# Kernel optimization log

Hardware: AMD Instinct MI355X
Metric: run time of the kernel (lower is better)

## Reference

```python
import jax, jax.numpy as jnp
import numpy as np

EPS = 1e-5
NUM_GRAPHS = 1000


def _glorot(key, shape):
    fan_in, fan_out = shape[1], shape[0]
    lim = float(np.sqrt(6.0 / (fan_in + fan_out)))
    return jax.random.uniform(key, shape, jnp.float32, -lim, lim)


def setup_inputs() -> dict:
    N, E, C, D, L = 100_000, 1_600_000, 10_000, 32, 4
    key = jax.random.key(0)
    ks = jax.random.split(key, 12)
    x = jax.random.normal(ks[0], (N, 2), jnp.float32)
    edge_index = jax.random.randint(ks[1], (2, E), 0, N)
    edge_attr = jax.random.normal(ks[2], (E, 1), jnp.float32)
    candidate_idxs = jax.random.randint(ks[3], (C,), 0, N)
    batch = jnp.sort(jax.random.randint(ks[4], (N,), 0, NUM_GRAPHS))
    lk = jax.random.split(ks[5], L)
    lk2 = jax.random.split(ks[6], L)
    return {
        "x": x,
        "edge_index": edge_index,
        "edge_attr": edge_attr,
        "candidate_idxs": candidate_idxs,
        "batch": batch,
        "lin_in_w": _glorot(ks[7], (D, 2)),
        "lin_in_b": jnp.zeros((D,), jnp.float32),
        "w1": jnp.stack([_glorot(lk[i], (D, 2 * D + 1)) for i in range(L)]),
        "b1": jnp.zeros((L, D), jnp.float32),
        "bn1_g": jnp.ones((L, D), jnp.float32),
        "bn1_b": jnp.zeros((L, D), jnp.float32),
        "w2": jnp.stack([_glorot(lk2[i], (D, D)) for i in range(L)]),
        "b2": jnp.zeros((L, D), jnp.float32),
        "bn2_g": jnp.ones((L, D), jnp.float32),
        "bn2_b": jnp.zeros((L, D), jnp.float32),
        "lin_out_w": _glorot(ks[8], (1, D)),
        "lin_out_b": jnp.zeros((), jnp.float32),
    }


def _batchnorm(m, g, b):
    # training-mode BatchNorm1d over the edge (row) axis, biased variance
    mu = jnp.mean(m, axis=0)
    var = jnp.mean(jnp.square(m - mu), axis=0)
    return (m - mu) * jax.lax.rsqrt(var + EPS) * g + b


def reference(x, edge_index, edge_attr, candidate_idxs, batch,
              lin_in_w, lin_in_b, w1, b1, bn1_g, bn1_b,
              w2, b2, bn2_g, bn2_b, lin_out_w, lin_out_b):
    N = x.shape[0]
    src, dst = edge_index[0], edge_index[1]  # x_j = x[src], x_i = x[dst]
    h = x @ lin_in_w.T + lin_in_b  # [N, D]
    for l in range(w1.shape[0]):
        msg = jnp.concatenate([h[dst], h[src], edge_attr], axis=-1)  # [E, 2D+1]
        m = jax.nn.relu(_batchnorm(msg @ w1[l].T + b1[l], bn1_g[l], bn1_b[l]))
        m = jax.nn.relu(_batchnorm(m @ w2[l].T + b2[l], bn2_g[l], bn2_b[l]))
        h = h + jax.ops.segment_sum(m, dst, num_segments=N)
    logits = (h[candidate_idxs] @ lin_out_w.T)[:, 0] + lin_out_b  # [C]
    seg = batch[candidate_idxs]
    mx = jax.ops.segment_max(logits, seg, num_segments=NUM_GRAPHS)
    mx = jnp.where(jnp.isfinite(mx), mx, 0.0)
    lse = mx + jnp.log(jax.ops.segment_sum(jnp.exp(logits - mx[seg]), seg,
                                           num_segments=NUM_GRAPHS))
    return logits - lse[seg]
```

## Files before the change

### kernel.cpp

```cpp
#include <hip/hip_runtime.h>
#include <stdint.h>

#define NGRAPH 1000

typedef __attribute__((ext_vector_type(8))) short short8;
typedef __attribute__((ext_vector_type(4))) float f32x4;

static __device__ __forceinline__ uint32_t pack2_bf16(float a, float b) {
  uint32_t ua = __float_as_uint(a), ub = __float_as_uint(b);
  ua = (ua + 0x7fffu + ((ua >> 16) & 1u)) >> 16;
  ub = (ub + 0x7fffu + ((ub >> 16) & 1u)) >> 16;
  return ua | (ub << 16);
}
static __device__ __forceinline__ unsigned short f2bf(float x) {
  uint32_t u = __float_as_uint(x);
  u = (u + 0x7fffu + ((u >> 16) & 1u)) >> 16;
  return (unsigned short)u;
}
static __device__ __forceinline__ float bf2f(unsigned short u) {
  return __uint_as_float(((uint32_t)u) << 16);
}
union frag_u { short8 v; uint32_t u[4]; };

__global__ __launch_bounds__(256) void k_prep(const float* __restrict__ w1,
                                              float* __restrict__ w1n,
                                              float* __restrict__ w1c) {
  int t = blockIdx.x * 256 + threadIdx.x;
  if (t < 4 * 2048) {
    int l = t >> 11, r = t & 2047, k = r >> 6, o = r & 63;
    w1n[t] = (o < 32) ? w1[l * 2080 + o * 65 + k]
                      : w1[l * 2080 + (o - 32) * 65 + (k + 32)];
  } else if (t < 4 * 2048 + 4 * 32) {
    int u = t - 4 * 2048;
    int l = u >> 5, d = u & 31;
    w1c[u] = w1[l * 2080 + d * 65 + 64];
  }
}

__global__ __launch_bounds__(256) void k_init(const float* __restrict__ x,
                                              const float* __restrict__ wi,
                                              const float* __restrict__ bi,
                                              float* __restrict__ h, int N) {
  int t = blockIdx.x * 256 + threadIdx.x;
  if (t >= N * 32) return;
  int n = t >> 5, d = t & 31;
  h[t] = fmaf(x[2 * n], wi[2 * d], fmaf(x[2 * n + 1], wi[2 * d + 1], bi[d]));
}

__global__ __launch_bounds__(256) void k_zero32(int* __restrict__ p, int n) {
  int t = blockIdx.x * 256 + threadIdx.x;
  if (t < n) p[t] = 0;
}

#define CHUNK 2048
__global__ __launch_bounds__(256) void k_bucket(const int* __restrict__ src,
                                                const int* __restrict__ dst,
                                                const float* __restrict__ ea,
                                                int* __restrict__ gcur,
                                                int* __restrict__ cnt,
                                                uint32_t* __restrict__ b0,
                                                uint32_t* __restrict__ b1,
                                                int E, int pstep, int cap) {
  __shared__ int lcnt[8], lbase[8];
  const int t = threadIdx.x;
  const int base = blockIdx.x * CHUNK;
  if (t < 8) lcnt[t] = 0;
  __syncthreads();
  int ps[8];
  uint32_t w0[8], w1[8];
#pragma unroll
  for (int j = 0; j < 8; j++) {
    int e = base + j * 256 + t;
    bool ok = e < E;
    int d = ok ? dst[e] : 0;
    int s = ok ? src[e] : 0;
    float eav = ok ? ea[e] : 0.f;
    int g = d / pstep;
    ps[j] = ok ? g : -1;
    if (ok) {
      int rank = atomicAdd(cnt + d, 1);
      w0[j] = ((uint32_t)s << 14) | (uint32_t)(rank & 16383);
      w1[j] = ((uint32_t)(d - g * pstep) << 16) | (uint32_t)f2bf(eav);
      atomicAdd(&lcnt[g], 1);
    }
  }
  __syncthreads();
  if (t < 8) lbase[t] = atomicAdd(&gcur[t], lcnt[t]);
  __syncthreads();
  if (t < 8) lcnt[t] = lbase[t];
  __syncthreads();
#pragma unroll
  for (int j = 0; j < 8; j++) {
    if (ps[j] >= 0) {
      int pos = atomicAdd(&lcnt[ps[j]], 1);
      if (pos < cap) {
        size_t idx = (size_t)ps[j] * cap + pos;
        b0[idx] = w0[j];
        b1[idx] = w1[j];
      }
    }
  }
}

__global__ __launch_bounds__(256) void k_scan1(const int* __restrict__ in,
                                               int* __restrict__ out,
                                               int* __restrict__ bsum, int n) {
  __shared__ int sh[256];
  const int t = threadIdx.x;
  const int idx = blockIdx.x * 1024 + t * 4;
  int v[4];
#pragma unroll
  for (int j = 0; j < 4; j++) v[j] = (idx + j < n) ? in[idx + j] : 0;
  int tsum = v[0] + v[1] + v[2] + v[3];
  sh[t] = tsum;
  __syncthreads();
#pragma unroll
  for (int ofs = 1; ofs < 256; ofs <<= 1) {
    int x = (t >= ofs) ? sh[t - ofs] : 0;
    __syncthreads();
    sh[t] += x;
    __syncthreads();
  }
  int run = sh[t] - tsum;
  if (t == 255) bsum[blockIdx.x] = sh[255];
#pragma unroll
  for (int j = 0; j < 4; j++) {
    if (idx + j < n) out[idx + j] = run;
    run += v[j];
  }
}
__global__ __launch_bounds__(256) void k_scan2(int* __restrict__ bsum, int nb) {
  __shared__ int sh[256];
  const int t = threadIdx.x;
  int val = (t < nb) ? bsum[t] : 0;
  sh[t] = val;
  __syncthreads();
#pragma unroll
  for (int ofs = 1; ofs < 256; ofs <<= 1) {
    int x = (t >= ofs) ? sh[t - ofs] : 0;
    __syncthreads();
    sh[t] += x;
    __syncthreads();
  }
  if (t < nb) bsum[t] = sh[t] - val;
}
__global__ __launch_bounds__(256) void k_scan3(int* __restrict__ rowptr,
                                               const int* __restrict__ bsum, int n) {
  int t = blockIdx.x * 256 + threadIdx.x;
  if (t >= n) return;
  rowptr[t] = rowptr[t] + bsum[t >> 10];
}

__global__ __launch_bounds__(256) void k_node(const float* __restrict__ h,
                                              const float* __restrict__ w1n,
                                              unsigned short* __restrict__ hAB, int N) {
  const int wid = (blockIdx.x * 256 + threadIdx.x) >> 6;
  const int lane = threadIdx.x & 63;
  if (wid >= N) return;
  const int n = __builtin_amdgcn_readfirstlane(wid);
  const float* hn = h + (size_t)n * 32;
  float acc = 0.f;
#pragma unroll
  for (int k = 0; k < 32; k++) acc = fmaf(hn[k], w1n[k * 64 + lane], acc);
  hAB[(size_t)n * 64 + lane] = f2bf(acc);
}

__global__ __launch_bounds__(256) void k_combine(
    const uint32_t* __restrict__ hAB, const uint32_t* __restrict__ b0,
    const uint32_t* __restrict__ b1, const int* __restrict__ gcur,
    const int* __restrict__ rowptr, const float* __restrict__ w1c,
    uint32_t* __restrict__ mpre, float* __restrict__ stats, int pstep, int cap) {
  const int t = threadIdx.x;
  const int r = t & 3;
  float ssum[8], ssq[8];
#pragma unroll
  for (int q = 0; q < 8; q++) { ssum[q] = 0.f; ssq[q] = 0.f; }
  float wc[8];
#pragma unroll
  for (int j = 0; j < 8; j++) wc[j] = w1c[8 * r + j];

  const int gstride = (gridDim.x * blockDim.x) >> 2;
  const int eg0 = (blockIdx.x * blockDim.x + t) >> 2;
  for (int g = 0; g < 8; g++) {
    const int len = gcur[g];
    const size_t o = (size_t)g * cap;
    for (int i = eg0; i < len; i += gstride) {
      const uint32_t w0 = b0[o + i];
      const uint32_t w1 = b1[o + i];
      const int vs = (int)(w0 >> 14);
      const int rank = (int)(w0 & 16383u);
      const int d = g * pstep + (int)(w1 >> 16);
      const float eav = bf2f((unsigned short)(w1 & 0xffffu));
      const int pos = rowptr[d] + rank;
      const uint4 av = *(const uint4*)(hAB + (size_t)d * 32 + r * 4);
      const uint4 bv = *(const uint4*)(hAB + (size_t)vs * 32 + 16 + r * 4);
      const uint32_t ad[4] = {av.x, av.y, av.z, av.w};
      const uint32_t bd[4] = {bv.x, bv.y, bv.z, bv.w};
      float m[8];
#pragma unroll
      for (int p = 0; p < 4; p++) {
        float a0 = __uint_as_float(ad[p] << 16), a1 = __uint_as_float(ad[p] & 0xffff0000u);
        float bb0 = __uint_as_float(bd[p] << 16), bb1 = __uint_as_float(bd[p] & 0xffff0000u);
        m[2 * p]     = a0 + fmaf(eav, wc[2 * p],     bb0);
        m[2 * p + 1] = a1 + fmaf(eav, wc[2 * p + 1], bb1);
      }
      uint4 out = make_uint4(pack2_bf16(m[0], m[1]), pack2_bf16(m[2], m[3]),
                             pack2_bf16(m[4], m[5]), pack2_bf16(m[6], m[7]));
      *(uint4*)(mpre + (size_t)pos * 16 + r * 4) = out;
#pragma unroll
      for (int q = 0; q < 8; q++) { ssum[q] += m[q]; ssq[q] = fmaf(m[q], m[q], ssq[q]); }
    }
  }
#pragma unroll
  for (int q = 0; q < 8; q++) {
#pragma unroll
    for (int msk = 4; msk <= 32; msk <<= 1) {
      ssum[q] += __shfl_xor(ssum[q], msk, 64);
      ssq[q]  += __shfl_xor(ssq[q],  msk, 64);
    }
  }
  __shared__ float red[4][64];
  const int lane = t & 63, wv = t >> 6;
  if (lane < 4) {
#pragma unroll
    for (int j = 0; j < 8; j++) {
      red[wv][lane * 8 + j]      = ssum[j];
      red[wv][32 + lane * 8 + j] = ssq[j];
    }
  }
  __syncthreads();
  if (t < 64)
    stats[(size_t)blockIdx.x * 64 + t] = red[0][t] + red[1][t] + red[2][t] + red[3][t];
}

__global__ __launch_bounds__(256) void k_finalize(const float* __restrict__ stats, int nblk, int E,
                                                  const float* __restrict__ g,
                                                  const float* __restrict__ bb,
                                                  float* __restrict__ ss) {
  const int q = blockIdx.x;
  const int t = threadIdx.x;
  double s0 = 0.0, s1 = 0.0;
  for (int i = t; i < nblk; i += 256) {
    s0 += (double)stats[(size_t)i * 64 + q];
    s1 += (double)stats[(size_t)i * 64 + 32 + q];
  }
  __shared__ double r0[256], r1[256];
  r0[t] = s0; r1[t] = s1;
  __syncthreads();
#pragma unroll
  for (int m = 128; m >= 1; m >>= 1) {
    if (t < m) { r0[t] += r0[t + m]; r1[t] += r1[t + m]; }
    __syncthreads();
  }
  if (t == 0) {
    double invE = 1.0 / (double)E;
    double mu = r0[0] * invE;
    double var = r1[0] * invE - mu * mu;
    if (var < 0.0) var = 0.0;
    double sc = (double)g[q] / sqrt(var + 1e-5);
    ss[q] = (float)sc;
    ss[32 + q] = (float)((double)bb[q] - mu * sc);
  }
}

__global__ __launch_bounds__(256) void k_gemm2m(
    uint32_t* __restrict__ mpre, const float* __restrict__ ss,
    const float* __restrict__ w2, float* __restrict__ stats, int E) {
  const int lane = threadIdx.x & 63;
  const int wv = threadIdx.x >> 6;
  const int row = lane & 15;
  const int kb = (lane >> 4) * 8;
  const int G = E >> 4;
  const int gstart = blockIdx.x * 4 + wv;
  const int gstride = gridDim.x * 4;

  float sc[8], sh[8];
#pragma unroll
  for (int j = 0; j < 8; j++) { sc[j] = ss[kb + j]; sh[j] = ss[32 + kb + j]; }

  frag_u b0, b1;
#pragma unroll
  for (int p = 0; p < 4; p++) {
    const float* wp0 = w2 + (size_t)row * 32 + kb + 2 * p;
    const float* wp1 = w2 + (size_t)(row + 16) * 32 + kb + 2 * p;
    b0.u[p] = pack2_bf16(wp0[0], wp0[1]);
    b1.u[p] = pack2_bf16(wp1[0], wp1[1]);
  }

  float sum0 = 0.f, sq0 = 0.f, sum1 = 0.f, sq1 = 0.f;
  unsigned short* mp16 = (unsigned short*)mpre;

  for (int g = gstart; g < G; g += gstride) {
    const int e0 = g << 4;
    const uint4 raw = *(const uint4*)(mpre + (size_t)(e0 + row) * 16 + (lane >> 4) * 4);
    float m[8];
    m[0] = __uint_as_float(raw.x << 16); m[1] = __uint_as_float(raw.x & 0xffff0000u);
    m[2] = __uint_as_float(raw.y << 16); m[3] = __uint_as_float(raw.y & 0xffff0000u);
    m[4] = __uint_as_float(raw.z << 16); m[5] = __uint_as_float(raw.z & 0xffff0000u);
    m[6] = __uint_as_float(raw.w << 16); m[7] = __uint_as_float(raw.w & 0xffff0000u);
    frag_u a;
#pragma unroll
    for (int p = 0; p < 4; p++) {
      float x0 = fmaxf(fmaf(m[2 * p],     sc[2 * p],     sh[2 * p]),     0.f);
      float x1 = fmaxf(fmaf(m[2 * p + 1], sc[2 * p + 1], sh[2 * p + 1]), 0.f);
      a.u[p] = pack2_bf16(x0, x1);
    }
    f32x4 z = {0.f, 0.f, 0.f, 0.f};
    f32x4 acc0 = __builtin_amdgcn_mfma_f32_16x16x32_bf16(a.v, b0.v, z, 0, 0, 0);
    f32x4 acc1 = __builtin_amdgcn_mfma_f32_16x16x32_bf16(a.v, b1.v, z, 0, 0, 0);
#pragma unroll
    for (int r = 0; r < 4; r++) {
      sum0 += acc0[r]; sq0 = fmaf(acc0[r], acc0[r], sq0);
      sum1 += acc1[r]; sq1 = fmaf(acc1[r], acc1[r], sq1);
      const size_t base = (size_t)(e0 + (lane >> 4) * 4 + r) * 32;
      mp16[base + row]      = f2bf(acc0[r]);
      mp16[base + row + 16] = f2bf(acc1[r]);
    }
  }

  sum0 += __shfl_xor(sum0, 16); sum0 += __shfl_xor(sum0, 32);
  sq0  += __shfl_xor(sq0, 16);  sq0  += __shfl_xor(sq0, 32);
  sum1 += __shfl_xor(sum1, 16); sum1 += __shfl_xor(sum1, 32);
  sq1  += __shfl_xor(sq1, 16);  sq1  += __shfl_xor(sq1, 32);
  __shared__ float red[4][64];
  if (lane < 16) {
    red[wv][row] = sum0;      red[wv][16 + row] = sum1;
    red[wv][32 + row] = sq0;  red[wv][48 + row] = sq1;
  }
  __syncthreads();
  if (threadIdx.x < 64) {
    int q = threadIdx.x;
    stats[(size_t)blockIdx.x * 64 + q] = red[0][q] + red[1][q] + red[2][q] + red[3][q];
  }
}

__global__ __launch_bounds__(256) void k_agg(
    const unsigned short* __restrict__ mp16, const int* __restrict__ rowptr,
    const int* __restrict__ cnt, const float* __restrict__ ss,
    float* __restrict__ h, int N) {
  const int n = blockIdx.x * 8 + (threadIdx.x >> 5);
  if (n >= N) return;
  const int d = threadIdx.x & 31;
  const int start = rowptr[n];
  const int deg = cnt[n];
  const float sc = ss[d], sh = ss[32 + d];
  const unsigned short* p = mp16 + (size_t)start * 32 + d;
  float acc = 0.f;
  int j = 0;
  for (; j + 2 <= deg; j += 2) {
    float x0 = bf2f(p[(size_t)j * 32]);
    float x1 = bf2f(p[(size_t)(j + 1) * 32]);
    acc += fmaxf(fmaf(x0, sc, sh), 0.f);
    acc += fmaxf(fmaf(x1, sc, sh), 0.f);
  }
  if (j < deg) {
    float x0 = bf2f(p[(size_t)j * 32]);
    acc += fmaxf(fmaf(x0, sc, sh), 0.f);
  }
  h[(size_t)n * 32 + d] += acc;
}

__global__ __launch_bounds__(256) void k_initseg(unsigned* __restrict__ segmax,
                                                 float* __restrict__ segsum) {
  int t = blockIdx.x * 256 + threadIdx.x;
  if (t < NGRAPH) { segmax[t] = 0u; segsum[t] = 0.f; }
}

__global__ __launch_bounds__(256) void k_logits(
    const float* __restrict__ h, const int* __restrict__ cand, const int* __restrict__ batch,
    const float* __restrict__ wout, const float* __restrict__ bout,
    float* __restrict__ logits, int* __restrict__ seg, unsigned* __restrict__ segmax, int C) {
  int t = blockIdx.x * 256 + threadIdx.x;
  if (t >= C) return;
  int node = cand[t];
  const float4* hp = (const float4*)(h + (size_t)node * 32);
  float acc = bout[0];
#pragma unroll
  for (int kc = 0; kc < 8; kc++) {
    float4 v = hp[kc];
    acc = fmaf(v.x, wout[kc * 4 + 0], acc);
    acc = fmaf(v.y, wout[kc * 4 + 1], acc);
    acc = fmaf(v.z, wout[kc * 4 + 2], acc);
    acc = fmaf(v.w, wout[kc * 4 + 3], acc);
  }
  logits[t] = acc;
  int s = batch[node];
  seg[t] = s;
  unsigned o = __float_as_uint(acc);
  o ^= (o >> 31) ? 0xFFFFFFFFu : 0x80000000u;
  atomicMax(segmax + s, o);
}

static __device__ __forceinline__ float o2f(unsigned o) {
  o ^= (o & 0x80000000u) ? 0x80000000u : 0xFFFFFFFFu;
  return __uint_as_float(o);
}

__global__ __launch_bounds__(256) void k_expsum(const float* __restrict__ logits,
                                                const int* __restrict__ seg,
                                                const unsigned* __restrict__ segmax,
                                                float* __restrict__ segsum, int C) {
  int t = blockIdx.x * 256 + threadIdx.x;
  if (t >= C) return;
  int s = seg[t];
  float mx = o2f(segmax[s]);
  atomicAdd(segsum + s, expf(logits[t] - mx));
}

__global__ __launch_bounds__(256) void k_out(const float* __restrict__ logits,
                                             const int* __restrict__ seg,
                                             const unsigned* __restrict__ segmax,
                                             const float* __restrict__ segsum,
                                             float* __restrict__ out, int C) {
  int t = blockIdx.x * 256 + threadIdx.x;
  if (t >= C) return;
  int s = seg[t];
  out[t] = logits[t] - (o2f(segmax[s]) + logf(segsum[s]));
}

extern "C" void kernel_launch(void* const* d_in, const int* in_sizes, int n_in,
                              void* d_out, int out_size, void* d_ws, size_t ws_size,
                              hipStream_t stream) {
  const float* x     = (const float*)d_in[0];
  const int*   eidx  = (const int*)d_in[1];
  const float* eattr = (const float*)d_in[2];
  const int*   cand  = (const int*)d_in[3];
  const int*   batch = (const int*)d_in[4];
  const float* wi    = (const float*)d_in[5];
  const float* bi    = (const float*)d_in[6];
  const float* w1    = (const float*)d_in[7];
  const float* g1    = (const float*)d_in[9];
  const float* bb1   = (const float*)d_in[10];
  const float* w2    = (const float*)d_in[11];
  const float* g2    = (const float*)d_in[13];
  const float* bb2   = (const float*)d_in[14];
  const float* wout  = (const float*)d_in[15];
  const float* bout  = (const float*)d_in[16];

  const int N = in_sizes[4];
  const int E = in_sizes[2];
  const int C = in_sizes[3];
  const int* src  = eidx;
  const int* dstp = eidx + E;

  char* ws = (char*)d_ws;
  size_t off = 0;
  auto carve = [&](size_t bytes) {
    void* p = ws + off;
    off = (off + bytes + 255) & ~(size_t)255;
    return p;
  };
  const int NBLK = 1024;
  const int pstep = (N + 7) / 8;
  const int cap = E / 8 + 8192;
  uint32_t* mpre   = (uint32_t*)carve((size_t)E * 64);
  float*    h      = (float*)carve((size_t)N * 32 * 4);
  uint32_t* hAB    = (uint32_t*)carve((size_t)N * 128);
  float*    w1n    = (float*)carve(4 * 2048 * 4);
  float*    w1c    = (float*)carve(4 * 32 * 4);
  float*    ss     = (float*)carve(64 * 4);
  float*    stats  = (float*)carve((size_t)NBLK * 64 * 4);
  int*      cnt    = (int*)carve((size_t)N * 4);
  int*      rowptr = (int*)carve((size_t)N * 4);
  int*      bsum   = (int*)carve(256 * 4);
  int*      gcur   = (int*)carve(8 * 4);
  uint32_t* b0     = (uint32_t*)carve((size_t)8 * cap * 4);
  uint32_t* b1buf  = (uint32_t*)carve((size_t)8 * cap * 4);
  float*    logits = (float*)carve((size_t)C * 4);
  int*      seg    = (int*)carve((size_t)C * 4);
  unsigned* segmax = (unsigned*)carve(NGRAPH * 4);
  float*    segsum = (float*)carve(NGRAPH * 4);
  (void)ws_size; (void)n_in; (void)out_size;

  const int nb1 = (N + 1023) / 1024;
  k_zero32<<<(N + 255) / 256, 256, 0, stream>>>(cnt, N);
  k_zero32<<<1, 256, 0, stream>>>(gcur, 8);
  k_bucket<<<(E + CHUNK - 1) / CHUNK, 256, 0, stream>>>(src, dstp, eattr, gcur, cnt,
                                                        b0, b1buf, E, pstep, cap);
  k_scan1<<<nb1, 256, 0, stream>>>(cnt, rowptr, bsum, N);
  k_scan2<<<1, 256, 0, stream>>>(bsum, nb1);
  k_scan3<<<(N + 255) / 256, 256, 0, stream>>>(rowptr, bsum, N);

  k_prep<<<33, 256, 0, stream>>>(w1, w1n, w1c);
  k_init<<<(N * 32 + 255) / 256, 256, 0, stream>>>(x, wi, bi, h, N);

  for (int l = 0; l < 4; l++) {
    k_node<<<(N * 64 + 255) / 256, 256, 0, stream>>>(h, w1n + l * 2048,
                                                     (unsigned short*)hAB, N);
    k_combine<<<NBLK, 256, 0, stream>>>(hAB, b0, b1buf, gcur, rowptr, w1c + l * 32,
                                        mpre, stats, pstep, cap);
    k_finalize<<<32, 256, 0, stream>>>(stats, NBLK, E, g1 + l * 32, bb1 + l * 32, ss);
    k_gemm2m<<<NBLK, 256, 0, stream>>>(mpre, ss, w2 + l * 1024, stats, E);
    k_finalize<<<32, 256, 0, stream>>>(stats, NBLK, E, g2 + l * 32, bb2 + l * 32, ss);
    k_agg<<<(N + 7) / 8, 256, 0, stream>>>((const unsigned short*)mpre, rowptr, cnt,
                                           ss, h, N);
  }

  k_initseg<<<(NGRAPH + 255) / 256, 256, 0, stream>>>(segmax, segsum);
  k_logits<<<(C + 255) / 256, 256, 0, stream>>>(h, cand, batch, wout, bout,
                                                logits, seg, segmax, C);
  k_expsum<<<(C + 255) / 256, 256, 0, stream>>>(logits, seg, segmax, segsum, C);
  k_out<<<(C + 255) / 256, 256, 0, stream>>>(logits, seg, segmax, segsum, (float*)d_out, C);
}
```

Baseline: 781.5 us.

## Fuse aggregation with next-layer node projection and split edge loop across half-waves

Merges the per-layer aggregation kernel with the following node projection (h @ W1 halves), so the updated h feeds the next layer's hAB computation without a separate launch and re-read. Each node now uses a full 64-lane wave, with the two halves splitting the edge loop and combining by shuffle. The k_bucket chunk is also halved, and the zero kernels are replaced with hipMemsetAsync. The fused kernel does more work per node (32 shuffles plus FMAs) and uses half-idle lanes for the h store.

```diff
diff --git a/kernel.cpp b/kernel.cpp
--- a/kernel.cpp
+++ b/kernel.cpp
@@ -47,12 +47,7 @@
   h[t] = fmaf(x[2 * n], wi[2 * d], fmaf(x[2 * n + 1], wi[2 * d + 1], bi[d]));
 }
 
-__global__ __launch_bounds__(256) void k_zero32(int* __restrict__ p, int n) {
-  int t = blockIdx.x * 256 + threadIdx.x;
-  if (t < n) p[t] = 0;
-}
-
-#define CHUNK 2048
+#define CHUNK 1024
 __global__ __launch_bounds__(256) void k_bucket(const int* __restrict__ src,
                                                 const int* __restrict__ dst,
                                                 const float* __restrict__ ea,
@@ -66,10 +61,10 @@
   const int base = blockIdx.x * CHUNK;
   if (t < 8) lcnt[t] = 0;
   __syncthreads();
-  int ps[8];
-  uint32_t w0[8], w1[8];
-#pragma unroll
-  for (int j = 0; j < 8; j++) {
+  int ps[4];
+  uint32_t w0[4], w1[4];
+#pragma unroll
+  for (int j = 0; j < 4; j++) {
     int e = base + j * 256 + t;
     bool ok = e < E;
     int d = ok ? dst[e] : 0;
@@ -90,7 +85,7 @@
   if (t < 8) lcnt[t] = lbase[t];
   __syncthreads();
 #pragma unroll
-  for (int j = 0; j < 8; j++) {
+  for (int j = 0; j < 4; j++) {
     if (ps[j] >= 0) {
       int pos = atomicAdd(&lcnt[ps[j]], 1);
       if (pos < cap) {
@@ -334,30 +329,34 @@
   }
 }
 
-__global__ __launch_bounds__(256) void k_agg(
+__global__ __launch_bounds__(256) void k_aggnode(
     const unsigned short* __restrict__ mp16, const int* __restrict__ rowptr,
     const int* __restrict__ cnt, const float* __restrict__ ss,
-    float* __restrict__ h, int N) {
-  const int n = blockIdx.x * 8 + (threadIdx.x >> 5);
-  if (n >= N) return;
-  const int d = threadIdx.x & 31;
+    float* __restrict__ h, const float* __restrict__ w1n,
+    unsigned short* __restrict__ hAB, int N, int last) {
+  const int wid = (blockIdx.x * 256 + threadIdx.x) >> 6;
+  const int lane = threadIdx.x & 63;
+  if (wid >= N) return;
+  const int n = __builtin_amdgcn_readfirstlane(wid);
+  const int d = lane & 31, half = lane >> 5;
   const int start = rowptr[n];
   const int deg = cnt[n];
-  const float sc = ss[d], sh = ss[32 + d];
+  const float scv = ss[d], shv = ss[32 + d];
   const unsigned short* p = mp16 + (size_t)start * 32 + d;
   float acc = 0.f;
-  int j = 0;
-  for (; j + 2 <= deg; j += 2) {
-    float x0 = bf2f(p[(size_t)j * 32]);
-    float x1 = bf2f(p[(size_t)(j + 1) * 32]);
-    acc += fmaxf(fmaf(x0, sc, sh), 0.f);
-    acc += fmaxf(fmaf(x1, sc, sh), 0.f);
-  }
-  if (j < deg) {
-    float x0 = bf2f(p[(size_t)j * 32]);
-    acc += fmaxf(fmaf(x0, sc, sh), 0.f);
-  }
-  h[(size_t)n * 32 + d] += acc;
+  for (int j = half; j < deg; j += 2) {
+    float x = bf2f(p[(size_t)j * 32]);
+    acc += fmaxf(fmaf(x, scv, shv), 0.f);
+  }
+  acc += __shfl_xor(acc, 32, 64);
+  const float hnew = h[(size_t)n * 32 + d] + acc;
+  if (lane < 32) h[(size_t)n * 32 + lane] = hnew;
+  if (last) return;
+  float acc2 = 0.f;
+#pragma unroll
+  for (int k = 0; k < 32; k++)
+    acc2 = fmaf(__shfl(hnew, k, 64), w1n[k * 64 + lane], acc2);
+  hAB[(size_t)n * 64 + lane] = f2bf(acc2);
 }
 
 __global__ __launch_bounds__(256) void k_initseg(unsigned* __restrict__ segmax,
@@ -473,8 +472,8 @@
   (void)ws_size; (void)n_in; (void)out_size;
 
   const int nb1 = (N + 1023) / 1024;
-  k_zero32<<<(N + 255) / 256, 256, 0, stream>>>(cnt, N);
-  k_zero32<<<1, 256, 0, stream>>>(gcur, 8);
+  hipMemsetAsync(cnt, 0, (size_t)N * 4, stream);
+  hipMemsetAsync(gcur, 0, 8 * 4, stream);
   k_bucket<<<(E + CHUNK - 1) / CHUNK, 256, 0, stream>>>(src, dstp, eattr, gcur, cnt,
                                                         b0, b1buf, E, pstep, cap);
   k_scan1<<<nb1, 256, 0, stream>>>(cnt, rowptr, bsum, N);
@@ -483,17 +482,17 @@
 
   k_prep<<<33, 256, 0, stream>>>(w1, w1n, w1c);
   k_init<<<(N * 32 + 255) / 256, 256, 0, stream>>>(x, wi, bi, h, N);
+  k_node<<<(N * 64 + 255) / 256, 256, 0, stream>>>(h, w1n, (unsigned short*)hAB, N);
 
   for (int l = 0; l < 4; l++) {
-    k_node<<<(N * 64 + 255) / 256, 256, 0, stream>>>(h, w1n + l * 2048,
-                                                     (unsigned short*)hAB, N);
     k_combine<<<NBLK, 256, 0, stream>>>(hAB, b0, b1buf, gcur, rowptr, w1c + l * 32,
                                         mpre, stats, pstep, cap);
     k_finalize<<<32, 256, 0, stream>>>(stats, NBLK, E, g1 + l * 32, bb1 + l * 32, ss);
     k_gemm2m<<<NBLK, 256, 0, stream>>>(mpre, ss, w2 + l * 1024, stats, E);
     k_finalize<<<32, 256, 0, stream>>>(stats, NBLK, E, g2 + l * 32, bb2 + l * 32, ss);
-    k_agg<<<(N + 7) / 8, 256, 0, stream>>>((const unsigned short*)mpre, rowptr, cnt,
-                                           ss, h, N);
+    k_aggnode<<<(N * 64 + 255) / 256, 256, 0, stream>>>(
+        (const unsigned short*)mpre, rowptr, cnt, ss, h,
+        w1n + (l + 1 < 4 ? (l + 1) * 2048 : 0), (unsigned short*)hAB, N, l == 3);
   }
 
   k_initseg<<<(NGRAPH + 255) / 256, 256, 0, stream>>>(segmax, segsum);
```

After: 826.7 us. 1.06x slower.
